# Performance work log

Hardware: AMD Instinct MI355X
Metric: run time of the kernel (lower is better)

Reference implementation:

```python
import jax, jax.numpy as jnp
import numpy as np

VOCAB, EMB_DIM, HIDDEN, NUM_CLASSES = 50000, 300, 1000, 5
B, MAX_LEN = 4096, 128


def setup_inputs() -> dict:
    key = jax.random.key(0)
    k1, k2, k3, k4, k5, k6, k7 = jax.random.split(key, 7)
    x = jax.random.randint(k1, (B, MAX_LEN), 0, VOCAB, dtype=jnp.int64)
    lengths = jnp.maximum(jax.random.randint(k2, (B,), 0, MAX_LEN, dtype=jnp.int64), 1)
    emb_table = jax.random.normal(k3, (VOCAB, EMB_DIM), dtype=jnp.float32) * 0.1
    W1 = jax.random.normal(k4, (2 * EMB_DIM, HIDDEN), dtype=jnp.float32) * (1.0 / np.sqrt(2 * EMB_DIM))
    b1 = jax.random.normal(k5, (HIDDEN,), dtype=jnp.float32) * 0.01
    W2 = jax.random.normal(k6, (HIDDEN, NUM_CLASSES), dtype=jnp.float32) * (1.0 / np.sqrt(HIDDEN))
    b2 = jax.random.normal(k7, (NUM_CLASSES,), dtype=jnp.float32) * 0.01
    return {"x": x, "lengths": lengths, "emb_table": emb_table,
            "W1": W1, "b1": b1, "W2": W2, "b2": b2}


def reference(x, lengths, emb_table, W1, b1, W2, b2):
    emb = emb_table[x]                                  # [B, L, D] gather
    mask = (jnp.arange(emb.shape[1])[None, :] < lengths[:, None])  # [B, L]
    m = mask[:, :, None].astype(emb.dtype)
    avg_pool = jnp.sum(emb * m, axis=1) / lengths[:, None].astype(emb.dtype)  # [B, D]
    neg_inf = jnp.finfo(emb.dtype).min
    max_pool = jnp.max(jnp.where(mask[:, :, None], emb, neg_inf), axis=1)     # [B, D]
    rep = jnp.concatenate([avg_pool, max_pool], axis=1)  # [B, 2D]
    hidden = jax.nn.relu(rep @ W1 + b1)                  # [B, 1000]
    logits = hidden @ W2 + b2                            # [B, C]
    return logits
```

## Files before the change

kernel.cpp:

```cpp
#include <hip/hip_runtime.h>
#include <float.h>
#include <stdint.h>

#define EMB_DIM  300
#define MAX_LEN  128
#define HIDDEN   1000
#define NCLS     5
#define VOCAB_SZ 50000
#define KPAD     640
#define NPAD     1024
#define EMBPAD   320

typedef float    f32x4   __attribute__((ext_vector_type(4)));
typedef __bf16   bf16x8  __attribute__((ext_vector_type(8)));
typedef unsigned short ushort8v __attribute__((ext_vector_type(8)));

#define EMB_CHUNKS (VOCAB_SZ * (EMBPAD / 8))
#define EMB_BLOCKS ((EMB_CHUNKS + 255) / 256)

__device__ __forceinline__ unsigned short f2bf(float f) {
    union { float f; uint32_t u; } v; v.f = f;
    uint32_t u = v.u;
    return (unsigned short)((u + 0x7FFFu + ((u >> 16) & 1u)) >> 16);
}
__device__ __forceinline__ float bf2f(unsigned short h) {
    union { uint32_t u; float f; } v; v.u = ((uint32_t)h) << 16;
    return v.f;
}

__global__ __launch_bounds__(256) void prep_all(
    const float* __restrict__ emb, unsigned short* __restrict__ embb,
    const float* __restrict__ W1, unsigned short* __restrict__ Bt,
    const float* __restrict__ W2, unsigned short* __restrict__ W2t,
    const float* __restrict__ b2, float* __restrict__ out,
    int M, int embBlocks)
{
    __shared__ float t[32][33];
    const int blk = blockIdx.x;

    if (blk < embBlocks) {
        const int i = blk * 256 + threadIdx.x;
        if (i >= EMB_CHUNKS) return;
        const int v  = i / 40;
        const int ch = i - v * 40;
        ushort8v o = {0, 0, 0, 0, 0, 0, 0, 0};
        if (ch < 38) {
            const float* src = emb + (size_t)v * EMB_DIM + ch * 8;
            const float4 f0 = *(const float4*)src;
            o[0] = f2bf(f0.x); o[1] = f2bf(f0.y); o[2] = f2bf(f0.z); o[3] = f2bf(f0.w);
            if (ch < 37) {
                const float4 f1 = *(const float4*)(src + 4);
                o[4] = f2bf(f1.x); o[5] = f2bf(f1.y); o[6] = f2bf(f1.z); o[7] = f2bf(f1.w);
            }
        }
        *(ushort8v*)(embb + (size_t)v * EMBPAD + ch * 8) = o;
        return;
    }
    const int pb = blk - embBlocks;
    if (pb < 640) {
        const int px = pb & 31, py = pb >> 5;
        const int tx = threadIdx.x & 31, ty = threadIdx.x >> 5;
        const int n0 = px * 32, k0 = py * 32;
        #pragma unroll
        for (int i = 0; i < 4; ++i) {
            int k = k0 + ty + i * 8, n = n0 + tx;
            t[ty + i * 8][tx] = (k < 600 && n < HIDDEN) ? W1[(size_t)k * HIDDEN + n] : 0.f;
        }
        __syncthreads();
        #pragma unroll
        for (int i = 0; i < 4; ++i) {
            int n = n0 + ty + i * 8, k = k0 + tx;
            Bt[(size_t)n * KPAD + k] = f2bf(t[tx][ty + i * 8]);
        }
        return;
    }
    const int pc = pb - 640;
    if (pc < 20) {
        const int i = pc * 256 + threadIdx.x;
        const int c = i >> 10, k = i & 1023;
        const float v = (k < HIDDEN) ? W2[(size_t)k * NCLS + c] : 0.f;
        W2t[(size_t)c * 1024 + k] = f2bf(v);
        return;
    }
    const int po = pc - 20;
    const int oi = po * 256 + threadIdx.x;
    if (oi < M * NCLS) out[oi] = b2[oi % NCLS];
}

__global__ __launch_bounds__(128) void pool_bf16(
    const int* __restrict__ x, const int* __restrict__ lengths,
    const unsigned short* __restrict__ embb, unsigned short* __restrict__ rep)
{
    const int b = blockIdx.x;
    const int t = threadIdx.x;

    __shared__ int sidx[MAX_LEN];
    {
        int v = x[b * MAX_LEN + t];
        sidx[t] = max(0, min(v, VOCAB_SZ - 1));
    }
    __syncthreads();

    unsigned short* rb = rep + (size_t)b * KPAD;

    if (t >= 75) {
        if (t < 85) {
            ushort4 z = {0, 0, 0, 0};
            *(ushort4*)(rb + 600 + (t - 75) * 4) = z;
        }
        return;
    }

    int L = lengths[b];
    L = max(1, min(L, MAX_LEN));

    const int d = t * 4;
    const unsigned short* base = embb + d;
    float4 s  = {0.f, 0.f, 0.f, 0.f};
    float4 mx = {-FLT_MAX, -FLT_MAX, -FLT_MAX, -FLT_MAX};

    int i = 0;
    for (; i + 4 <= L; i += 4) {
        const ushort4 u0 = *(const ushort4*)(base + (size_t)sidx[i]     * EMBPAD);
        const ushort4 u1 = *(const ushort4*)(base + (size_t)sidx[i + 1] * EMBPAD);
        const ushort4 u2 = *(const ushort4*)(base + (size_t)sidx[i + 2] * EMBPAD);
        const ushort4 u3 = *(const ushort4*)(base + (size_t)sidx[i + 3] * EMBPAD);
        float a0 = bf2f(u0.x), a1 = bf2f(u0.y), a2 = bf2f(u0.z), a3 = bf2f(u0.w);
        float b0 = bf2f(u1.x), b1v = bf2f(u1.y), b2v = bf2f(u1.z), b3 = bf2f(u1.w);
        float c0 = bf2f(u2.x), c1 = bf2f(u2.y), c2 = bf2f(u2.z), c3 = bf2f(u2.w);
        float e0 = bf2f(u3.x), e1 = bf2f(u3.y), e2 = bf2f(u3.z), e3 = bf2f(u3.w);
        s.x += (a0 + b0) + (c0 + e0);
        s.y += (a1 + b1v) + (c1 + e1);
        s.z += (a2 + b2v) + (c2 + e2);
        s.w += (a3 + b3) + (c3 + e3);
        mx.x = fmaxf(mx.x, fmaxf(fmaxf(a0, b0), fmaxf(c0, e0)));
        mx.y = fmaxf(mx.y, fmaxf(fmaxf(a1, b1v), fmaxf(c1, e1)));
        mx.z = fmaxf(mx.z, fmaxf(fmaxf(a2, b2v), fmaxf(c2, e2)));
        mx.w = fmaxf(mx.w, fmaxf(fmaxf(a3, b3), fmaxf(c3, e3)));
    }
    for (; i < L; ++i) {
        const ushort4 u = *(const ushort4*)(base + (size_t)sidx[i] * EMBPAD);
        float a0 = bf2f(u.x), a1 = bf2f(u.y), a2 = bf2f(u.z), a3 = bf2f(u.w);
        s.x += a0; s.y += a1; s.z += a2; s.w += a3;
        mx.x = fmaxf(mx.x, a0); mx.y = fmaxf(mx.y, a1);
        mx.z = fmaxf(mx.z, a2); mx.w = fmaxf(mx.w, a3);
    }

    const float inv = 1.0f / (float)L;
    ushort4 av, mv;
    av.x = f2bf(s.x * inv); av.y = f2bf(s.y * inv);
    av.z = f2bf(s.z * inv); av.w = f2bf(s.w * inv);
    mv.x = f2bf(mx.x); mv.y = f2bf(mx.y); mv.z = f2bf(mx.z); mv.w = f2bf(mx.w);
    *(ushort4*)(rb + d)       = av;
    *(ushort4*)(rb + 300 + d) = mv;
}

__global__ __launch_bounds__(128) void pool_f32(
    const int* __restrict__ x, const int* __restrict__ lengths,
    const float* __restrict__ emb, unsigned short* __restrict__ rep)
{
    const int b = blockIdx.x;
    const int t = threadIdx.x;

    __shared__ int sidx[MAX_LEN];
    sidx[t] = x[b * MAX_LEN + t];
    __syncthreads();

    unsigned short* rb = rep + (size_t)b * KPAD;

    if (t >= 75) {
        if (t < 85) {
            ushort4 z = {0, 0, 0, 0};
            *(ushort4*)(rb + 600 + (t - 75) * 4) = z;
        }
        return;
    }

    int L = lengths[b];
    L = max(1, min(L, MAX_LEN));

    const int d = t * 4;
    float4 s  = {0.f, 0.f, 0.f, 0.f};
    float4 mx = {-FLT_MAX, -FLT_MAX, -FLT_MAX, -FLT_MAX};

    for (int i = 0; i < L; ++i) {
        int idx = max(0, min(sidx[i], VOCAB_SZ - 1));
        const float4 v = *(const float4*)(emb + (size_t)idx * EMB_DIM + d);
        s.x += v.x; s.y += v.y; s.z += v.z; s.w += v.w;
        mx.x = fmaxf(mx.x, v.x); mx.y = fmaxf(mx.y, v.y);
        mx.z = fmaxf(mx.z, v.z); mx.w = fmaxf(mx.w, v.w);
    }

    const float inv = 1.0f / (float)L;
    ushort4 av, mv;
    av.x = f2bf(s.x * inv); av.y = f2bf(s.y * inv);
    av.z = f2bf(s.z * inv); av.w = f2bf(s.w * inv);
    mv.x = f2bf(mx.x); mv.y = f2bf(mx.y); mv.z = f2bf(mx.z); mv.w = f2bf(mx.w);
    *(ushort4*)(rb + d)       = av;
    *(ushort4*)(rb + 300 + d) = mv;
}

#define BM 128
#define BN 128
#define BK 64

__global__ __launch_bounds__(256, 2) void gemm1p(
    const unsigned short* __restrict__ A,
    const unsigned short* __restrict__ Bt,
    const float* __restrict__ bias,
    const unsigned short* __restrict__ W2t,
    float* __restrict__ out,
    int M)
{
    __shared__ unsigned short As[2][BM * BK];
    __shared__ unsigned short Bs[2][BN * BK];

    const int tid  = threadIdx.x;
    const int wv   = tid >> 6;
    const int lane = tid & 63;
    const int bm   = blockIdx.y * BM;
    const int bn   = blockIdx.x * BN;
    const int wr   = (wv & 1) * 64;
    const int wc   = (wv >> 1) * 64;

    f32x4 acc[4][4] = {};

    auto stage = [&](int buf, int k0) {
        #pragma unroll
        for (int j = 0; j < 4; ++j) {
            const int ci  = (wv * 4 + j) * 64 + lane;
            const int row = ci >> 3, c = ci & 7;
            __builtin_amdgcn_global_load_lds(
                A + (size_t)(bm + row) * KPAD + k0 + c * 8,
                &As[buf][(wv * 4 + j) * 512], 16, 0, 0);
        }
        #pragma unroll
        for (int j = 0; j < 4; ++j) {
            const int ci  = (wv * 4 + j) * 64 + lane;
            const int row = ci >> 3, c = ci & 7;
            __builtin_amdgcn_global_load_lds(
                Bt + (size_t)(bn + row) * KPAD + k0 + c * 8,
                &Bs[buf][(wv * 4 + j) * 512], 16, 0, 0);
        }
    };

    stage(0, 0);
    int cur = 0;
    const int q = lane >> 4, r16 = lane & 15;

    #pragma unroll 1
    for (int it = 0; it < KPAD / BK; ++it) {
        __syncthreads();
        if (it + 1 < KPAD / BK) stage(cur ^ 1, (it + 1) * BK);

        #pragma unroll
        for (int ks = 0; ks < BK; ks += 32) {
            bf16x8 af[4], bfr[4];
            #pragma unroll
            for (int mi = 0; mi < 4; ++mi)
                af[mi] = *(const bf16x8*)&As[cur][(wr + mi * 16 + r16) * BK + ks + q * 8];
            #pragma unroll
            for (int nj = 0; nj < 4; ++nj)
                bfr[nj] = *(const bf16x8*)&Bs[cur][(wc + nj * 16 + r16) * BK + ks + q * 8];
            #pragma unroll
            for (int mi = 0; mi < 4; ++mi)
                #pragma unroll
                for (int nj = 0; nj < 4; ++nj)
                    acc[mi][nj] = __builtin_amdgcn_mfma_f32_16x16x32_bf16(
                        af[mi], bfr[nj], acc[mi][nj], 0, 0, 0);
        }
        cur ^= 1;
    }

    float bv[4], w2v[4][NCLS];
    #pragma unroll
    for (int nj = 0; nj < 4; ++nj) {
        const int n = bn + wc + nj * 16 + r16;
        if (n < HIDDEN) {
            bv[nj] = bias[n];
            #pragma unroll
            for (int c = 0; c < NCLS; ++c) w2v[nj][c] = bf2f(W2t[c * 1024 + n]);
        } else {
            bv[nj] = 0.f;
            #pragma unroll
            for (int c = 0; c < NCLS; ++c) w2v[nj][c] = 0.f;
        }
    }

    __syncthreads();
    float* pl = (float*)As;

    #pragma unroll
    for (int mi = 0; mi < 4; ++mi) {
        #pragma unroll
        for (int r = 0; r < 4; ++r) {
            float p[NCLS] = {0.f, 0.f, 0.f, 0.f, 0.f};
            #pragma unroll
            for (int nj = 0; nj < 4; ++nj) {
                float h = fmaxf(acc[mi][nj][r] + bv[nj], 0.f);
                #pragma unroll
                for (int c = 0; c < NCLS; ++c) p[c] += h * w2v[nj][c];
            }
            #pragma unroll
            for (int off = 1; off < 16; off <<= 1)
                #pragma unroll
                for (int c = 0; c < NCLS; ++c)
                    p[c] += __shfl_xor(p[c], off, 64);
            if (r16 == 0) {
                const int lr = mi * 16 + q * 4 + r;
                #pragma unroll
                for (int c = 0; c < NCLS; ++c)
                    pl[(wv * 64 + lr) * NCLS + c] = p[c];
            }
        }
    }
    __syncthreads();

    for (int e = tid; e < BM * NCLS; e += 256) {
        const int lr = e / NCLS, c = e - lr * NCLS;
        float v;
        if (lr < 64) v = pl[(0 * 64 + lr)      * NCLS + c] + pl[(2 * 64 + lr)      * NCLS + c];
        else         v = pl[(1 * 64 + lr - 64) * NCLS + c] + pl[(3 * 64 + lr - 64) * NCLS + c];
        atomicAdd(out + (size_t)(bm + lr) * NCLS + c, v);
    }
}

extern "C" void kernel_launch(void* const* d_in, const int* in_sizes, int n_in,
                              void* d_out, int out_size, void* d_ws, size_t ws_size,
                              hipStream_t stream)
{
    const int*   x       = (const int*)d_in[0];
    const int*   lengths = (const int*)d_in[1];
    const float* emb     = (const float*)d_in[2];
    const float* W1      = (const float*)d_in[3];
    const float* b1      = (const float*)d_in[4];
    const float* W2      = (const float*)d_in[5];
    const float* b2      = (const float*)d_in[6];
    float*       out     = (float*)d_out;

    const int B = in_sizes[1];

    unsigned short* rep  = (unsigned short*)d_ws;
    unsigned short* w1t  = rep + (size_t)B * KPAD;
    unsigned short* w2t  = w1t + (size_t)NPAD * KPAD;
    unsigned short* embb = w2t + (size_t)NCLS * 1024;

    const size_t need = ((size_t)B * KPAD + (size_t)NPAD * KPAD + NCLS * 1024
                         + (size_t)VOCAB_SZ * EMBPAD) * 2;

    const bool useBf16  = (ws_size >= need);
    const int  embBlks  = useBf16 ? EMB_BLOCKS : 0;
    const int  outBlks  = (B * NCLS + 255) / 256;

    prep_all<<<embBlks + 660 + outBlks, 256, 0, stream>>>(
        emb, embb, W1, w1t, W2, w2t, b2, out, B, embBlks);

    if (useBf16) {
        pool_bf16<<<B, 128, 0, stream>>>(x, lengths, embb, rep);
    } else {
        pool_f32<<<B, 128, 0, stream>>>(x, lengths, emb, rep);
    }

    dim3 g1(NPAD / BN, B / BM);
    gemm1p<<<g1, 256, 0, stream>>>(rep, w1t, b1, w2t, out, B);
}
```

Before: 161.0 us.

## Fuse pooling into prep kernel and gather fp32 embeddings directly

Drops the per-call conversion of the whole 50000x300 embedding table to bf16 and instead gathers fp32 rows directly during pooling. Pooling is merged into the weight-prep kernel, with two batch rows per 256-thread block, which removes one kernel launch and lets weight transposition overlap with pooling. In exchange, each gathered row now reads twice as many bytes (fp32 instead of bf16), but the full-table read and write is gone.

```diff
diff --git a/kernel.cpp b/kernel.cpp
--- a/kernel.cpp
+++ b/kernel.cpp
@@ -9,14 +9,9 @@
 #define VOCAB_SZ 50000
 #define KPAD     640
 #define NPAD     1024
-#define EMBPAD   320
 
 typedef float    f32x4   __attribute__((ext_vector_type(4)));
 typedef __bf16   bf16x8  __attribute__((ext_vector_type(8)));
-typedef unsigned short ushort8v __attribute__((ext_vector_type(8)));
-
-#define EMB_CHUNKS (VOCAB_SZ * (EMBPAD / 8))
-#define EMB_BLOCKS ((EMB_CHUNKS + 255) / 256)
 
 __device__ __forceinline__ unsigned short f2bf(float f) {
     union { float f; uint32_t u; } v; v.f = f;
@@ -28,176 +23,110 @@
     return v.f;
 }
 
-__global__ __launch_bounds__(256) void prep_all(
-    const float* __restrict__ emb, unsigned short* __restrict__ embb,
+__global__ __launch_bounds__(256) void fused_prep_pool(
+    const int* __restrict__ x, const int* __restrict__ lengths,
+    const float* __restrict__ emb,
     const float* __restrict__ W1, unsigned short* __restrict__ Bt,
     const float* __restrict__ W2, unsigned short* __restrict__ W2t,
     const float* __restrict__ b2, float* __restrict__ out,
-    int M, int embBlocks)
+    unsigned short* __restrict__ rep,
+    int M, int poolBlocks)
 {
-    __shared__ float t[32][33];
+    __shared__ float tsh[32][33];
+    __shared__ int   sidx[2][MAX_LEN];
     const int blk = blockIdx.x;
-
-    if (blk < embBlocks) {
-        const int i = blk * 256 + threadIdx.x;
-        if (i >= EMB_CHUNKS) return;
-        const int v  = i / 40;
-        const int ch = i - v * 40;
-        ushort8v o = {0, 0, 0, 0, 0, 0, 0, 0};
-        if (ch < 38) {
-            const float* src = emb + (size_t)v * EMB_DIM + ch * 8;
-            const float4 f0 = *(const float4*)src;
-            o[0] = f2bf(f0.x); o[1] = f2bf(f0.y); o[2] = f2bf(f0.z); o[3] = f2bf(f0.w);
-            if (ch < 37) {
-                const float4 f1 = *(const float4*)(src + 4);
-                o[4] = f2bf(f1.x); o[5] = f2bf(f1.y); o[6] = f2bf(f1.z); o[7] = f2bf(f1.w);
+    const int tid = threadIdx.x;
+
+    if (blk < poolBlocks) {
+        const int half = tid >> 7;
+        const int t    = tid & 127;
+        const int b    = blk * 2 + half;
+        {
+            int v = x[b * MAX_LEN + t];
+            sidx[half][t] = max(0, min(v, VOCAB_SZ - 1));
+        }
+        __syncthreads();
+
+        unsigned short* rb = rep + (size_t)b * KPAD;
+
+        if (t >= 75) {
+            if (t < 85) {
+                ushort4 z = {0, 0, 0, 0};
+                *(ushort4*)(rb + 600 + (t - 75) * 4) = z;
             }
-        }
-        *(ushort8v*)(embb + (size_t)v * EMBPAD + ch * 8) = o;
+            return;
+        }
+
+        int L = lengths[b];
+        L = max(1, min(L, MAX_LEN));
+
+        const int d = t * 4;
+        const float* base = emb + d;
+        const int* si = sidx[half];
+        float4 s  = {0.f, 0.f, 0.f, 0.f};
+        float4 mx = {-FLT_MAX, -FLT_MAX, -FLT_MAX, -FLT_MAX};
+
+        int i = 0;
+        for (; i + 4 <= L; i += 4) {
+            const float4 a = *(const float4*)(base + (size_t)si[i]     * EMB_DIM);
+            const float4 c = *(const float4*)(base + (size_t)si[i + 1] * EMB_DIM);
+            const float4 e = *(const float4*)(base + (size_t)si[i + 2] * EMB_DIM);
+            const float4 g = *(const float4*)(base + (size_t)si[i + 3] * EMB_DIM);
+            s.x += (a.x + c.x) + (e.x + g.x);
+            s.y += (a.y + c.y) + (e.y + g.y);
+            s.z += (a.z + c.z) + (e.z + g.z);
+            s.w += (a.w + c.w) + (e.w + g.w);
+            mx.x = fmaxf(mx.x, fmaxf(fmaxf(a.x, c.x), fmaxf(e.x, g.x)));
+            mx.y = fmaxf(mx.y, fmaxf(fmaxf(a.y, c.y), fmaxf(e.y, g.y)));
+            mx.z = fmaxf(mx.z, fmaxf(fmaxf(a.z, c.z), fmaxf(e.z, g.z)));
+            mx.w = fmaxf(mx.w, fmaxf(fmaxf(a.w, c.w), fmaxf(e.w, g.w)));
+        }
+        for (; i < L; ++i) {
+            const float4 a = *(const float4*)(base + (size_t)si[i] * EMB_DIM);
+            s.x += a.x; s.y += a.y; s.z += a.z; s.w += a.w;
+            mx.x = fmaxf(mx.x, a.x); mx.y = fmaxf(mx.y, a.y);
+            mx.z = fmaxf(mx.z, a.z); mx.w = fmaxf(mx.w, a.w);
+        }
+
+        const float inv = 1.0f / (float)L;
+        ushort4 av, mv;
+        av.x = f2bf(s.x * inv); av.y = f2bf(s.y * inv);
+        av.z = f2bf(s.z * inv); av.w = f2bf(s.w * inv);
+        mv.x = f2bf(mx.x); mv.y = f2bf(mx.y); mv.z = f2bf(mx.z); mv.w = f2bf(mx.w);
+        *(ushort4*)(rb + d)       = av;
+        *(ushort4*)(rb + 300 + d) = mv;
         return;
     }
-    const int pb = blk - embBlocks;
+
+    const int pb = blk - poolBlocks;
     if (pb < 640) {
         const int px = pb & 31, py = pb >> 5;
-        const int tx = threadIdx.x & 31, ty = threadIdx.x >> 5;
+        const int tx = tid & 31, ty = tid >> 5;
         const int n0 = px * 32, k0 = py * 32;
         #pragma unroll
         for (int i = 0; i < 4; ++i) {
             int k = k0 + ty + i * 8, n = n0 + tx;
-            t[ty + i * 8][tx] = (k < 600 && n < HIDDEN) ? W1[(size_t)k * HIDDEN + n] : 0.f;
+            tsh[ty + i * 8][tx] = (k < 600 && n < HIDDEN) ? W1[(size_t)k * HIDDEN + n] : 0.f;
         }
         __syncthreads();
         #pragma unroll
         for (int i = 0; i < 4; ++i) {
             int n = n0 + ty + i * 8, k = k0 + tx;
-            Bt[(size_t)n * KPAD + k] = f2bf(t[tx][ty + i * 8]);
+            Bt[(size_t)n * KPAD + k] = f2bf(tsh[tx][ty + i * 8]);
         }
         return;
     }
     const int pc = pb - 640;
     if (pc < 20) {
-        const int i = pc * 256 + threadIdx.x;
+        const int i = pc * 256 + tid;
         const int c = i >> 10, k = i & 1023;
         const float v = (k < HIDDEN) ? W2[(size_t)k * NCLS + c] : 0.f;
         W2t[(size_t)c * 1024 + k] = f2bf(v);
         return;
     }
     const int po = pc - 20;
-    const int oi = po * 256 + threadIdx.x;
+    const int oi = po * 256 + tid;
     if (oi < M * NCLS) out[oi] = b2[oi % NCLS];
-}
-
-__global__ __launch_bounds__(128) void pool_bf16(
-    const int* __restrict__ x, const int* __restrict__ lengths,
-    const unsigned short* __restrict__ embb, unsigned short* __restrict__ rep)
-{
-    const int b = blockIdx.x;
-    const int t = threadIdx.x;
-
-    __shared__ int sidx[MAX_LEN];
-    {
-        int v = x[b * MAX_LEN + t];
-        sidx[t] = max(0, min(v, VOCAB_SZ - 1));
-    }
-    __syncthreads();
-
-    unsigned short* rb = rep + (size_t)b * KPAD;
-
-    if (t >= 75) {
-        if (t < 85) {
-            ushort4 z = {0, 0, 0, 0};
-            *(ushort4*)(rb + 600 + (t - 75) * 4) = z;
-        }
-        return;
-    }
-
-    int L = lengths[b];
-    L = max(1, min(L, MAX_LEN));
-
-    const int d = t * 4;
-    const unsigned short* base = embb + d;
-    float4 s  = {0.f, 0.f, 0.f, 0.f};
-    float4 mx = {-FLT_MAX, -FLT_MAX, -FLT_MAX, -FLT_MAX};
-
-    int i = 0;
-    for (; i + 4 <= L; i += 4) {
-        const ushort4 u0 = *(const ushort4*)(base + (size_t)sidx[i]     * EMBPAD);
-        const ushort4 u1 = *(const ushort4*)(base + (size_t)sidx[i + 1] * EMBPAD);
-        const ushort4 u2 = *(const ushort4*)(base + (size_t)sidx[i + 2] * EMBPAD);
-        const ushort4 u3 = *(const ushort4*)(base + (size_t)sidx[i + 3] * EMBPAD);
-        float a0 = bf2f(u0.x), a1 = bf2f(u0.y), a2 = bf2f(u0.z), a3 = bf2f(u0.w);
-        float b0 = bf2f(u1.x), b1v = bf2f(u1.y), b2v = bf2f(u1.z), b3 = bf2f(u1.w);
-        float c0 = bf2f(u2.x), c1 = bf2f(u2.y), c2 = bf2f(u2.z), c3 = bf2f(u2.w);
-        float e0 = bf2f(u3.x), e1 = bf2f(u3.y), e2 = bf2f(u3.z), e3 = bf2f(u3.w);
-        s.x += (a0 + b0) + (c0 + e0);
-        s.y += (a1 + b1v) + (c1 + e1);
-        s.z += (a2 + b2v) + (c2 + e2);
-        s.w += (a3 + b3) + (c3 + e3);
-        mx.x = fmaxf(mx.x, fmaxf(fmaxf(a0, b0), fmaxf(c0, e0)));
-        mx.y = fmaxf(mx.y, fmaxf(fmaxf(a1, b1v), fmaxf(c1, e1)));
-        mx.z = fmaxf(mx.z, fmaxf(fmaxf(a2, b2v), fmaxf(c2, e2)));
-        mx.w = fmaxf(mx.w, fmaxf(fmaxf(a3, b3), fmaxf(c3, e3)));
-    }
-    for (; i < L; ++i) {
-        const ushort4 u = *(const ushort4*)(base + (size_t)sidx[i] * EMBPAD);
-        float a0 = bf2f(u.x), a1 = bf2f(u.y), a2 = bf2f(u.z), a3 = bf2f(u.w);
-        s.x += a0; s.y += a1; s.z += a2; s.w += a3;
-        mx.x = fmaxf(mx.x, a0); mx.y = fmaxf(mx.y, a1);
-        mx.z = fmaxf(mx.z, a2); mx.w = fmaxf(mx.w, a3);
-    }
-
-    const float inv = 1.0f / (float)L;
-    ushort4 av, mv;
-    av.x = f2bf(s.x * inv); av.y = f2bf(s.y * inv);
-    av.z = f2bf(s.z * inv); av.w = f2bf(s.w * inv);
-    mv.x = f2bf(mx.x); mv.y = f2bf(mx.y); mv.z = f2bf(mx.z); mv.w = f2bf(mx.w);
-    *(ushort4*)(rb + d)       = av;
-    *(ushort4*)(rb + 300 + d) = mv;
-}
-
-__global__ __launch_bounds__(128) void pool_f32(
-    const int* __restrict__ x, const int* __restrict__ lengths,
-    const float* __restrict__ emb, unsigned short* __restrict__ rep)
-{
-    const int b = blockIdx.x;
-    const int t = threadIdx.x;
-
-    __shared__ int sidx[MAX_LEN];
-    sidx[t] = x[b * MAX_LEN + t];
-    __syncthreads();
-
-    unsigned short* rb = rep + (size_t)b * KPAD;
-
-    if (t >= 75) {
-        if (t < 85) {
-            ushort4 z = {0, 0, 0, 0};
-            *(ushort4*)(rb + 600 + (t - 75) * 4) = z;
-        }
-        return;
-    }
-
-    int L = lengths[b];
-    L = max(1, min(L, MAX_LEN));
-
-    const int d = t * 4;
-    float4 s  = {0.f, 0.f, 0.f, 0.f};
-    float4 mx = {-FLT_MAX, -FLT_MAX, -FLT_MAX, -FLT_MAX};
-
-    for (int i = 0; i < L; ++i) {
-        int idx = max(0, min(sidx[i], VOCAB_SZ - 1));
-        const float4 v = *(const float4*)(emb + (size_t)idx * EMB_DIM + d);
-        s.x += v.x; s.y += v.y; s.z += v.z; s.w += v.w;
-        mx.x = fmaxf(mx.x, v.x); mx.y = fmaxf(mx.y, v.y);
-        mx.z = fmaxf(mx.z, v.z); mx.w = fmaxf(mx.w, v.w);
-    }
-
-    const float inv = 1.0f / (float)L;
-    ushort4 av, mv;
-    av.x = f2bf(s.x * inv); av.y = f2bf(s.y * inv);
-    av.z = f2bf(s.z * inv); av.w = f2bf(s.w * inv);
-    mv.x = f2bf(mx.x); mv.y = f2bf(mx.y); mv.z = f2bf(mx.z); mv.w = f2bf(mx.w);
-    *(ushort4*)(rb + d)       = av;
-    *(ushort4*)(rb + 300 + d) = mv;
 }
 
 #define BM 128
@@ -340,26 +269,16 @@
 
     const int B = in_sizes[1];
 
-    unsigned short* rep  = (unsigned short*)d_ws;
-    unsigned short* w1t  = rep + (size_t)B * KPAD;
-    unsigned short* w2t  = w1t + (size_t)NPAD * KPAD;
-    unsigned short* embb = w2t + (size_t)NCLS * 1024;
-
-    const size_t need = ((size_t)B * KPAD + (size_t)NPAD * KPAD + NCLS * 1024
-                         + (size_t)VOCAB_SZ * EMBPAD) * 2;
-
-    const bool useBf16  = (ws_size >= need);
-    const int  embBlks  = useBf16 ? EMB_BLOCKS : 0;
-    const int  outBlks  = (B * NCLS + 255) / 256;
-
-    prep_all<<<embBlks + 660 + outBlks, 256, 0, stream>>>(
-        emb, embb, W1, w1t, W2, w2t, b2, out, B, embBlks);
-
-    if (useBf16) {
-        pool_bf16<<<B, 128, 0, stream>>>(x, lengths, embb, rep);
-    } else {
-        pool_f32<<<B, 128, 0, stream>>>(x, lengths, emb, rep);
-    }
+    unsigned short* rep = (unsigned short*)d_ws;
+    unsigned short* w1t = rep + (size_t)B * KPAD;
+    unsigned short* w2t = w1t + (size_t)NPAD * KPAD;
+
+    const int poolBlks = B / 2;
+    const int outBlks  = (B * NCLS + 255) / 256;
+    const int grid     = poolBlks + 640 + 20 + outBlks;
+
+    fused_prep_pool<<<grid, 256, 0, stream>>>(
+        x, lengths, emb, W1, w1t, W2, w2t, b2, out, rep, B, poolBlks);
 
     dim3 g1(NPAD / BN, B / BM);
     gemm1p<<<g1, 256, 0, stream>>>(rep, w1t, b1, w2t, out, B);
```

New measurement: 167.1 us. 3.8% more time.

## Pool four rows per block with 16-byte gathers and padded rep layout

Applied to the files above, without the earlier changes.

The bf16 pooling kernel now handles four batch rows per 256-thread block, one wavefront per row. Each lane loads 8 bf16 values (16 bytes) per gathered embedding row instead of 4, halving the number of gather instructions. The rep layout places max-pool at offset 320 so that 16-byte aligned stores cover the padded embedding columns. W1's transposed weights are remapped to match this 300+20-pad layout. Idle lanes (24 of 64 per wave) and the assumption that B is divisible by 4 are the trade-offs.

```diff
diff --git a/kernel.cpp b/kernel.cpp
--- a/kernel.cpp
+++ b/kernel.cpp
@@ -35,11 +35,12 @@
     const float* __restrict__ b2, float* __restrict__ out,
     int M, int embBlocks)
 {
-    __shared__ float t[32][33];
+    __shared__ float tsh[32][33];
     const int blk = blockIdx.x;
+    const int tid = threadIdx.x;
 
     if (blk < embBlocks) {
-        const int i = blk * 256 + threadIdx.x;
+        const int i = blk * 256 + tid;
         if (i >= EMB_CHUNKS) return;
         const int v  = i / 40;
         const int ch = i - v * 40;
@@ -59,37 +60,103 @@
     const int pb = blk - embBlocks;
     if (pb < 640) {
         const int px = pb & 31, py = pb >> 5;
-        const int tx = threadIdx.x & 31, ty = threadIdx.x >> 5;
+        const int tx = tid & 31, ty = tid >> 5;
         const int n0 = px * 32, k0 = py * 32;
         #pragma unroll
         for (int i = 0; i < 4; ++i) {
-            int k = k0 + ty + i * 8, n = n0 + tx;
-            t[ty + i * 8][tx] = (k < 600 && n < HIDDEN) ? W1[(size_t)k * HIDDEN + n] : 0.f;
+            const int k = k0 + ty + i * 8, n = n0 + tx;
+            const int r = (k < 300) ? k : ((k >= 320 && k < 620) ? (k - 20) : -1);
+            tsh[ty + i * 8][tx] = (r >= 0 && n < HIDDEN) ? W1[(size_t)r * HIDDEN + n] : 0.f;
         }
         __syncthreads();
         #pragma unroll
         for (int i = 0; i < 4; ++i) {
-            int n = n0 + ty + i * 8, k = k0 + tx;
-            Bt[(size_t)n * KPAD + k] = f2bf(t[tx][ty + i * 8]);
+            const int n = n0 + ty + i * 8, k = k0 + tx;
+            Bt[(size_t)n * KPAD + k] = f2bf(tsh[tx][ty + i * 8]);
         }
         return;
     }
     const int pc = pb - 640;
     if (pc < 20) {
-        const int i = pc * 256 + threadIdx.x;
+        const int i = pc * 256 + tid;
         const int c = i >> 10, k = i & 1023;
         const float v = (k < HIDDEN) ? W2[(size_t)k * NCLS + c] : 0.f;
         W2t[(size_t)c * 1024 + k] = f2bf(v);
         return;
     }
     const int po = pc - 20;
-    const int oi = po * 256 + threadIdx.x;
+    const int oi = po * 256 + tid;
     if (oi < M * NCLS) out[oi] = b2[oi % NCLS];
 }
 
-__global__ __launch_bounds__(128) void pool_bf16(
+__global__ __launch_bounds__(256) void pool_w16(
     const int* __restrict__ x, const int* __restrict__ lengths,
     const unsigned short* __restrict__ embb, unsigned short* __restrict__ rep)
+{
+    __shared__ int sidx[4 * MAX_LEN];
+    const int blk = blockIdx.x;
+    const int tid = threadIdx.x;
+
+    {
+        int v0 = x[blk * 512 + tid];
+        int v1 = x[blk * 512 + tid + 256];
+        sidx[tid]       = max(0, min(v0, VOCAB_SZ - 1));
+        sidx[tid + 256] = max(0, min(v1, VOCAB_SZ - 1));
+    }
+    __syncthreads();
+
+    const int w = tid >> 6;
+    const int l = tid & 63;
+    const int b = blk * 4 + w;
+
+    int L = lengths[b];
+    L = max(1, min(L, MAX_LEN));
+
+    if (l >= 40) return;
+
+    const int d = l * 8;
+    const unsigned short* base = embb + d;
+    const int* si = sidx + w * MAX_LEN;
+
+    float s[8], mx[8];
+    #pragma unroll
+    for (int e = 0; e < 8; ++e) { s[e] = 0.f; mx[e] = -FLT_MAX; }
+
+    int i = 0;
+    for (; i + 4 <= L; i += 4) {
+        const ushort8v u0 = *(const ushort8v*)(base + (size_t)si[i]     * EMBPAD);
+        const ushort8v u1 = *(const ushort8v*)(base + (size_t)si[i + 1] * EMBPAD);
+        const ushort8v u2 = *(const ushort8v*)(base + (size_t)si[i + 2] * EMBPAD);
+        const ushort8v u3 = *(const ushort8v*)(base + (size_t)si[i + 3] * EMBPAD);
+        #pragma unroll
+        for (int e = 0; e < 8; ++e) {
+            const float f0 = bf2f(u0[e]), f1 = bf2f(u1[e]);
+            const float f2 = bf2f(u2[e]), f3 = bf2f(u3[e]);
+            s[e]  += (f0 + f1) + (f2 + f3);
+            mx[e]  = fmaxf(mx[e], fmaxf(fmaxf(f0, f1), fmaxf(f2, f3)));
+        }
+    }
+    for (; i < L; ++i) {
+        const ushort8v u = *(const ushort8v*)(base + (size_t)si[i] * EMBPAD);
+        #pragma unroll
+        for (int e = 0; e < 8; ++e) {
+            const float f = bf2f(u[e]);
+            s[e] += f;
+            mx[e] = fmaxf(mx[e], f);
+        }
+    }
+
+    const float inv = 1.0f / (float)L;
+    ushort8v av, mv;
+    #pragma unroll
+    for (int e = 0; e < 8; ++e) { av[e] = f2bf(s[e] * inv); mv[e] = f2bf(mx[e]); }
+    *(ushort8v*)(rep + (size_t)b * KPAD + d)       = av;
+    *(ushort8v*)(rep + (size_t)b * KPAD + 320 + d) = mv;
+}
+
+__global__ __launch_bounds__(128) void pool_f32_fb(
+    const int* __restrict__ x, const int* __restrict__ lengths,
+    const float* __restrict__ emb, unsigned short* __restrict__ rep)
 {
     const int b = blockIdx.x;
     const int t = threadIdx.x;
@@ -104,9 +171,12 @@
     unsigned short* rb = rep + (size_t)b * KPAD;
 
     if (t >= 75) {
-        if (t < 85) {
+        if (t < 80) {
             ushort4 z = {0, 0, 0, 0};
-            *(ushort4*)(rb + 600 + (t - 75) * 4) = z;
+            *(ushort4*)(rb + 300 + (t - 75) * 4) = z;
+        } else if (t < 85) {
+            ushort4 z = {0, 0, 0, 0};
+            *(ushort4*)(rb + 620 + (t - 80) * 4) = z;
         }
         return;
     }
@@ -115,35 +185,15 @@
     L = max(1, min(L, MAX_LEN));
 
     const int d = t * 4;
-    const unsigned short* base = embb + d;
+    const float* base = emb + d;
     float4 s  = {0.f, 0.f, 0.f, 0.f};
     float4 mx = {-FLT_MAX, -FLT_MAX, -FLT_MAX, -FLT_MAX};
 
-    int i = 0;
-    for (; i + 4 <= L; i += 4) {
-        const ushort4 u0 = *(const ushort4*)(base + (size_t)sidx[i]     * EMBPAD);
-        const ushort4 u1 = *(const ushort4*)(base + (size_t)sidx[i + 1] * EMBPAD);
-        const ushort4 u2 = *(const ushort4*)(base + (size_t)sidx[i + 2] * EMBPAD);
-        const ushort4 u3 = *(const ushort4*)(base + (size_t)sidx[i + 3] * EMBPAD);
-        float a0 = bf2f(u0.x), a1 = bf2f(u0.y), a2 = bf2f(u0.z), a3 = bf2f(u0.w);
-        float b0 = bf2f(u1.x), b1v = bf2f(u1.y), b2v = bf2f(u1.z), b3 = bf2f(u1.w);
-        float c0 = bf2f(u2.x), c1 = bf2f(u2.y), c2 = bf2f(u2.z), c3 = bf2f(u2.w);
-        float e0 = bf2f(u3.x), e1 = bf2f(u3.y), e2 = bf2f(u3.z), e3 = bf2f(u3.w);
-        s.x += (a0 + b0) + (c0 + e0);
-        s.y += (a1 + b1v) + (c1 + e1);
-        s.z += (a2 + b2v) + (c2 + e2);
-        s.w += (a3 + b3) + (c3 + e3);
-        mx.x = fmaxf(mx.x, fmaxf(fmaxf(a0, b0), fmaxf(c0, e0)));
-        mx.y = fmaxf(mx.y, fmaxf(fmaxf(a1, b1v), fmaxf(c1, e1)));
-        mx.z = fmaxf(mx.z, fmaxf(fmaxf(a2, b2v), fmaxf(c2, e2)));
-        mx.w = fmaxf(mx.w, fmaxf(fmaxf(a3, b3), fmaxf(c3, e3)));
-    }
-    for (; i < L; ++i) {
-        const ushort4 u = *(const ushort4*)(base + (size_t)sidx[i] * EMBPAD);
-        float a0 = bf2f(u.x), a1 = bf2f(u.y), a2 = bf2f(u.z), a3 = bf2f(u.w);
-        s.x += a0; s.y += a1; s.z += a2; s.w += a3;
-        mx.x = fmaxf(mx.x, a0); mx.y = fmaxf(mx.y, a1);
-        mx.z = fmaxf(mx.z, a2); mx.w = fmaxf(mx.w, a3);
+    for (int i = 0; i < L; ++i) {
+        const float4 a = *(const float4*)(base + (size_t)sidx[i] * EMB_DIM);
+        s.x += a.x; s.y += a.y; s.z += a.z; s.w += a.w;
+        mx.x = fmaxf(mx.x, a.x); mx.y = fmaxf(mx.y, a.y);
+        mx.z = fmaxf(mx.z, a.z); mx.w = fmaxf(mx.w, a.w);
     }
 
     const float inv = 1.0f / (float)L;
@@ -152,52 +202,7 @@
     av.z = f2bf(s.z * inv); av.w = f2bf(s.w * inv);
     mv.x = f2bf(mx.x); mv.y = f2bf(mx.y); mv.z = f2bf(mx.z); mv.w = f2bf(mx.w);
     *(ushort4*)(rb + d)       = av;
-    *(ushort4*)(rb + 300 + d) = mv;
-}
-
-__global__ __launch_bounds__(128) void pool_f32(
-    const int* __restrict__ x, const int* __restrict__ lengths,
-    const float* __restrict__ emb, unsigned short* __restrict__ rep)
-{
-    const int b = blockIdx.x;
-    const int t = threadIdx.x;
-
-    __shared__ int sidx[MAX_LEN];
-    sidx[t] = x[b * MAX_LEN + t];
-    __syncthreads();
-
-    unsigned short* rb = rep + (size_t)b * KPAD;
-
-    if (t >= 75) {
-        if (t < 85) {
-            ushort4 z = {0, 0, 0, 0};
-            *(ushort4*)(rb + 600 + (t - 75) * 4) = z;
-        }
-        return;
-    }
-
-    int L = lengths[b];
-    L = max(1, min(L, MAX_LEN));
-
-    const int d = t * 4;
-    float4 s  = {0.f, 0.f, 0.f, 0.f};
-    float4 mx = {-FLT_MAX, -FLT_MAX, -FLT_MAX, -FLT_MAX};
-
-    for (int i = 0; i < L; ++i) {
-        int idx = max(0, min(sidx[i], VOCAB_SZ - 1));
-        const float4 v = *(const float4*)(emb + (size_t)idx * EMB_DIM + d);
-        s.x += v.x; s.y += v.y; s.z += v.z; s.w += v.w;
-        mx.x = fmaxf(mx.x, v.x); mx.y = fmaxf(mx.y, v.y);
-        mx.z = fmaxf(mx.z, v.z); mx.w = fmaxf(mx.w, v.w);
-    }
-
-    const float inv = 1.0f / (float)L;
-    ushort4 av, mv;
-    av.x = f2bf(s.x * inv); av.y = f2bf(s.y * inv);
-    av.z = f2bf(s.z * inv); av.w = f2bf(s.w * inv);
-    mv.x = f2bf(mx.x); mv.y = f2bf(mx.y); mv.z = f2bf(mx.z); mv.w = f2bf(mx.w);
-    *(ushort4*)(rb + d)       = av;
-    *(ushort4*)(rb + 300 + d) = mv;
+    *(ushort4*)(rb + 320 + d) = mv;
 }
 
 #define BM 128
@@ -348,17 +353,17 @@
     const size_t need = ((size_t)B * KPAD + (size_t)NPAD * KPAD + NCLS * 1024
                          + (size_t)VOCAB_SZ * EMBPAD) * 2;
 
-    const bool useBf16  = (ws_size >= need);
-    const int  embBlks  = useBf16 ? EMB_BLOCKS : 0;
-    const int  outBlks  = (B * NCLS + 255) / 256;
+    const bool useBf16 = (ws_size >= need);
+    const int  embBlks = useBf16 ? EMB_BLOCKS : 0;
+    const int  outBlks = (B * NCLS + 255) / 256;
 
     prep_all<<<embBlks + 660 + outBlks, 256, 0, stream>>>(
         emb, embb, W1, w1t, W2, w2t, b2, out, B, embBlks);
 
     if (useBf16) {
-        pool_bf16<<<B, 128, 0, stream>>>(x, lengths, embb, rep);
+        pool_w16<<<B / 4, 256, 0, stream>>>(x, lengths, embb, rep);
     } else {
-        pool_f32<<<B, 128, 0, stream>>>(x, lengths, emb, rep);
+        pool_f32_fb<<<B, 128, 0, stream>>>(x, lengths, emb, rep);
     }
 
     dim3 g1(NPAD / BN, B / BM);
```

Result: slower. 165.0 us (+2.5%).
